# Performance work log

Measured on AMD Instinct MI355X. Metric: run time of the kernel, lower is better.

Reference implementation:

```python
import jax, jax.numpy as jnp
import numpy as np

B, S, D, H = 2, 2048, 1024, 16
DEPTH = D // H


def setup_inputs() -> dict:
    key = jax.random.key(0)
    ks = jax.random.split(key, 12)
    s = 0.02
    inp = {
        "query": jax.random.normal(ks[0], (B, S, D), jnp.float32),
        "key": jax.random.normal(ks[1], (B, S, D), jnp.float32),
        "value": jax.random.normal(ks[2], (B, S, D), jnp.float32),
        # causal mask: 1.0 where attention is disallowed (j > i)
        "mask": jnp.triu(jnp.ones((S, S), jnp.float32), k=1)[None, None, :, :],
        "wq": jax.random.normal(ks[3], (D, D), jnp.float32) * s,
        "bq": jnp.zeros((D,), jnp.float32),
        "wk": jax.random.normal(ks[4], (D, D), jnp.float32) * s,
        "bk": jnp.zeros((D,), jnp.float32),
        "wv": jax.random.normal(ks[5], (D, D), jnp.float32) * s,
        "bv": jnp.zeros((D,), jnp.float32),
        "wo": jax.random.normal(ks[6], (D, D), jnp.float32) * s,
        "bo": jnp.zeros((D,), jnp.float32),
    }
    return inp


def _split_heads(x):
    # [B,S,D] -> [B,H,S,depth]
    b, s, _ = x.shape
    return x.reshape(b, s, H, DEPTH).transpose(0, 2, 1, 3)


def reference(query, key, value, mask, wq, bq, wk, bk, wv, bv, wo, bo):
    q = _split_heads(query @ wq + bq)
    k = _split_heads(key @ wk + bk)
    v = _split_heads(value @ wv + bv)
    scale = jnp.sqrt(jnp.asarray(DEPTH, jnp.float32))
    scores = jnp.einsum("bhqd,bhkd->bhqk", q, k) / scale  # [B,H,S,S]
    scores = scores + mask * (-1e9)
    attn = jax.nn.softmax(scores, axis=-1)
    out = jnp.einsum("bhqk,bhkd->bhqd", attn, v)
    out = out.transpose(0, 2, 1, 3).reshape(query.shape[0], query.shape[1], D)
    return out @ wo + bo
```

## Files before the change

kernel.cpp:

```cpp
#include <hip/hip_runtime.h>
#include <hip/hip_bf16.h>
#include <stdint.h>
#include <math.h>

typedef float f32x4  __attribute__((ext_vector_type(4)));
typedef float f32x16 __attribute__((ext_vector_type(16)));
typedef short s16x8  __attribute__((ext_vector_type(8)));
typedef unsigned u32x4 __attribute__((ext_vector_type(4)));

#define SEQ     2048
#define DMODEL  1024
#define MROWS   4096
#define NHEAD   16

__device__ __forceinline__ unsigned short f2b(float x) {
    union { float f; unsigned u; } un; un.f = x;
    unsigned r = un.u + 0x7FFFu + ((un.u >> 16) & 1u);
    return (unsigned short)(r >> 16);
}

__device__ __forceinline__ unsigned cvtpk(float lo, float hi_) {
    unsigned r;
    asm("v_cvt_pk_bf16_f32 %0, %1, %2" : "=v"(r) : "v"(lo), "v"(hi_));
    return r;
}

#define EXP2(x) __builtin_amdgcn_exp2f(x)

__device__ __forceinline__ void g2l16(const void* g, void* l) {
    __builtin_amdgcn_global_load_lds(
        (const __attribute__((address_space(1))) unsigned int*)g,
        (__attribute__((address_space(3))) unsigned int*)l,
        16, 0, 0);
}

__global__ __launch_bounds__(256) void wtrans_kernel(
    const float* __restrict__ w0, const float* __restrict__ w1,
    const float* __restrict__ w2, const float* __restrict__ w3,
    unsigned short* __restrict__ wt)
{
    const int z = blockIdx.z;
    const float* w = z == 0 ? w0 : z == 1 ? w1 : z == 2 ? w2 : w3;
    __shared__ float t[32][33];
    const int bx = blockIdx.x * 32;
    const int by = blockIdx.y * 32;
    const int tx = threadIdx.x, ty = threadIdx.y;
    #pragma unroll
    for (int i = 0; i < 4; ++i)
        t[ty + i*8][tx] = w[(size_t)(by + ty + i*8) * DMODEL + bx + tx];
    __syncthreads();
    unsigned short* o = wt + (size_t)z * ((size_t)DMODEL * DMODEL);
    #pragma unroll
    for (int i = 0; i < 4; ++i) {
        int nrel = ty + i*8, krel = tx;
        o[(size_t)(bx + nrel) * DMODEL + by + krel] = f2b(t[krel][nrel]);
    }
}

__global__ __launch_bounds__(256, 3) void gemm_qkv_kernel(
    const float* __restrict__ qf, const float* __restrict__ kf, const float* __restrict__ vf,
    const unsigned short* __restrict__ wtbase,
    const float* __restrict__ b0, const float* __restrict__ b1, const float* __restrict__ b2,
    unsigned short* __restrict__ qh, unsigned short* __restrict__ kh,
    unsigned short* __restrict__ vT)
{
    const int mode = blockIdx.z;
    const float* Af = mode == 0 ? qf : mode == 1 ? kf : vf;
    const unsigned short* Bt = wtbase + (size_t)mode * ((size_t)DMODEL * DMODEL);
    const float* bias = mode == 0 ? b0 : mode == 1 ? b1 : b2;

    __shared__ unsigned short As[128 * 64];
    __shared__ unsigned short Bs[128 * 64];

    const int tid = threadIdx.x;
    const int lane = tid & 63, wid = tid >> 6;
    const int ll = lane & 15, lg = lane >> 4;
    const int mb = blockIdx.x * 128, nb = blockIdx.y * 128;
    const int wr = wid >> 1, wc = wid & 1;

    f32x4 acc[4][4] = {};
    f32x4 stgA[8];

    auto issueA = [&](int kb) {
        #pragma unroll
        for (int it = 0; it < 4; ++it) {
            int ci = it * 256 + tid;
            int r = ci >> 3;
            int cbs = ((ci & 7) * 16) ^ ((r & 7) << 4);
            const float* src = Af + (size_t)(mb + r) * DMODEL + kb + (cbs >> 1);
            stgA[2 * it]     = *(const f32x4*)src;
            stgA[2 * it + 1] = *(const f32x4*)(src + 4);
        }
    };

    issueA(0);

    for (int kb = 0; kb < DMODEL; kb += 64) {
        __syncthreads();
        #pragma unroll
        for (int it = 0; it < 4; ++it) {
            u32x4 w = { cvtpk(stgA[2*it][0],   stgA[2*it][1]),
                        cvtpk(stgA[2*it][2],   stgA[2*it][3]),
                        cvtpk(stgA[2*it+1][0], stgA[2*it+1][1]),
                        cvtpk(stgA[2*it+1][2], stgA[2*it+1][3]) };
            *(u32x4*)((char*)As + (it * 256 + tid) * 16) = w;
        }
        #pragma unroll
        for (int it = 0; it < 4; ++it) {
            int ci = it * 256 + tid;
            int r = ci >> 3;
            int cbs = ((ci & 7) * 16) ^ ((r & 7) << 4);
            g2l16((const char*)Bt + ((size_t)(nb + r) * DMODEL + kb) * 2 + cbs,
                  (char*)Bs + (it * 256 + wid * 64) * 16);
        }
        __syncthreads();
        if (kb + 64 < DMODEL) issueA(kb + 64);

        #pragma unroll
        for (int kk = 0; kk < 2; ++kk) {
            s16x8 af[4], bfr[4];
            #pragma unroll
            for (int m = 0; m < 4; ++m) {
                int row = wr * 64 + m * 16 + ll;
                int cbyte = (kk * 64 + lg * 16) ^ ((row & 7) << 4);
                af[m] = *(const s16x8*)((const char*)As + row * 128 + cbyte);
            }
            #pragma unroll
            for (int n = 0; n < 4; ++n) {
                int row = wc * 64 + n * 16 + ll;
                int cbyte = (kk * 64 + lg * 16) ^ ((row & 7) << 4);
                bfr[n] = *(const s16x8*)((const char*)Bs + row * 128 + cbyte);
            }
            #pragma unroll
            for (int m = 0; m < 4; ++m)
                #pragma unroll
                for (int n = 0; n < 4; ++n)
                    acc[m][n] = __builtin_amdgcn_mfma_f32_16x16x32_bf16(af[m], bfr[n], acc[m][n], 0, 0, 0);
        }
    }

    #pragma unroll
    for (int m = 0; m < 4; ++m) {
        int grow0 = mb + wr * 64 + m * 16 + lg * 4;
        #pragma unroll
        for (int n = 0; n < 4; ++n) {
            int col = nb + wc * 64 + n * 16 + ll;
            float bc = bias[col];
            f32x4 v = acc[m][n];
            if (mode == 2) {
                int b = grow0 >> 11, s0 = grow0 & 2047;
                int h = col >> 6, d = col & 63;
                ushort4 pk;
                pk.x = f2b(v[0] + bc); pk.y = f2b(v[1] + bc);
                pk.z = f2b(v[2] + bc); pk.w = f2b(v[3] + bc);
                *(ushort4*)(vT + ((size_t)((b * NHEAD + h) * 64 + d) << 11) + s0) = pk;
            } else {
                unsigned short* dst = (mode == 0) ? qh : kh;
                float scl = (mode == 0) ? 0.125f * 1.44269504089f : 1.0f;
                int b = grow0 >> 11, s0 = grow0 & 2047;
                int h = col >> 6, d = col & 63;
                #pragma unroll
                for (int r = 0; r < 4; ++r)
                    dst[((size_t)(b * NHEAD + h) * SEQ + s0 + r) * 64 + d] = f2b((v[r] + bc) * scl);
            }
        }
    }
}

__global__ __launch_bounds__(256, 2) void gemm_o_kernel(
    const unsigned short* __restrict__ Ap,
    const unsigned short* __restrict__ Bt,
    const float* __restrict__ bias,
    float* __restrict__ outF)
{
    constexpr int TM = 64;
    constexpr int WM = TM / 2;
    constexpr int MT = WM / 16;

    __shared__ unsigned short As[TM * 64];
    __shared__ unsigned short Bs[128 * 64];

    const int tid = threadIdx.x;
    const int lane = tid & 63, wid = tid >> 6;
    const int ll = lane & 15, lg = lane >> 4;
    const int mb = blockIdx.x * TM, nb = blockIdx.y * 128;
    const int wr = wid >> 1, wc = wid & 1;

    f32x4 acc[MT][4] = {};
    u32x4 stgA[2], stgB[4];

    auto issueA = [&](int kb) {
        #pragma unroll
        for (int it = 0; it < 2; ++it) {
            int ci = it * 256 + tid;
            int r = ci >> 3;
            int cbs = ((ci & 7) * 16) ^ ((r & 7) << 4);
            stgA[it] = *(const u32x4*)((const char*)Ap + ((size_t)(mb + r) * DMODEL + kb) * 2 + cbs);
        }
    };
    auto issueB = [&](int kb) {
        #pragma unroll
        for (int it = 0; it < 4; ++it) {
            int ci = it * 256 + tid;
            int r = ci >> 3;
            int cbs = ((ci & 7) * 16) ^ ((r & 7) << 4);
            stgB[it] = *(const u32x4*)((const char*)Bt + ((size_t)(nb + r) * DMODEL + kb) * 2 + cbs);
        }
    };

    issueA(0);
    issueB(0);

    for (int kb = 0; kb < DMODEL; kb += 64) {
        __syncthreads();
        #pragma unroll
        for (int it = 0; it < 2; ++it)
            *(u32x4*)((char*)As + (it * 256 + tid) * 16) = stgA[it];
        #pragma unroll
        for (int it = 0; it < 4; ++it)
            *(u32x4*)((char*)Bs + (it * 256 + tid) * 16) = stgB[it];
        __syncthreads();
        if (kb + 64 < DMODEL) { issueA(kb + 64); issueB(kb + 64); }

        #pragma unroll
        for (int kk = 0; kk < 2; ++kk) {
            s16x8 af[MT], bfr[4];
            #pragma unroll
            for (int m = 0; m < MT; ++m) {
                int row = wr * WM + m * 16 + ll;
                int cbyte = (kk * 64 + lg * 16) ^ ((row & 7) << 4);
                af[m] = *(const s16x8*)((const char*)As + row * 128 + cbyte);
            }
            #pragma unroll
            for (int n = 0; n < 4; ++n) {
                int row = wc * 64 + n * 16 + ll;
                int cbyte = (kk * 64 + lg * 16) ^ ((row & 7) << 4);
                bfr[n] = *(const s16x8*)((const char*)Bs + row * 128 + cbyte);
            }
            #pragma unroll
            for (int m = 0; m < MT; ++m)
                #pragma unroll
                for (int n = 0; n < 4; ++n)
                    acc[m][n] = __builtin_amdgcn_mfma_f32_16x16x32_bf16(af[m], bfr[n], acc[m][n], 0, 0, 0);
        }
    }

    #pragma unroll
    for (int m = 0; m < MT; ++m) {
        int grow0 = mb + wr * WM + m * 16 + lg * 4;
        #pragma unroll
        for (int n = 0; n < 4; ++n) {
            int col = nb + wc * 64 + n * 16 + ll;
            float bc = bias[col];
            f32x4 v = acc[m][n];
            #pragma unroll
            for (int r = 0; r < 4; ++r)
                outF[(size_t)(grow0 + r) * DMODEL + col] = v[r] + bc;
        }
    }
}

__global__ __launch_bounds__(256, 3) void attn_kernel(
    const unsigned short* __restrict__ qh, const unsigned short* __restrict__ kh,
    const unsigned short* __restrict__ vT, unsigned short* __restrict__ attnout)
{
    const int bid = blockIdx.x;
    const int bh = bid & 31;
    const int j  = 31 - (bid >> 5);
    const int qb = j * 64;
    const int nss = (j >> 1) + 1;

    const unsigned short* Q = qh + (size_t)bh * (SEQ * 64);
    const unsigned short* K = kh + (size_t)bh * (SEQ * 64);
    const unsigned short* V = vT + (size_t)bh * (64 * SEQ);

    __shared__ char lds[32768];
    char* Kb = lds;
    char* Vb = lds + 16384;

    const int tid = threadIdx.x, lane = tid & 63, wid = tid >> 6;
    const int l31 = lane & 31, hi = lane >> 5;
    const int qhf = wid & 1;
    const int par = wid >> 1;
    const int qrow = qb + qhf * 32 + l31;

    s16x8 aq[4];
    {
        const unsigned short* qp = Q + (size_t)qrow * 64 + hi * 8;
        #pragma unroll
        for (int u = 0; u < 4; ++u)
            aq[u] = *(const s16x8*)(qp + u * 16);
    }

    f32x16 oc0 = {}, oc1 = {};
    float mrow = -1e30f, lrow = 0.f;

    u32x4 stg[8];
    auto issue = [&](int kb) {
        #pragma unroll
        for (int it = 0; it < 4; ++it) {
            int ci = it * 256 + tid;
            int r = ci >> 3;
            int sb = ((ci & 7) * 16) ^ ((r & 7) << 4);
            stg[it] = *(const u32x4*)((const char*)K + ((size_t)(kb + r) * 64) * 2 + sb);
        }
        #pragma unroll
        for (int it = 0; it < 4; ++it) {
            int ci = it * 256 + tid;
            int d = ci >> 4;
            int sb = ((ci & 15) * 16) ^ ((d & 15) << 4);
            stg[4 + it] = *(const u32x4*)((const char*)V + (size_t)d * (SEQ * 2) + (size_t)kb * 2 + sb);
        }
    };

    issue(0);

    for (int ss = 0; ss < nss; ++ss) {
        const int kb = ss * 128;
        __syncthreads();
        #pragma unroll
        for (int it = 0; it < 8; ++it)
            *(u32x4*)(lds + it * 4096 + tid * 16) = stg[it];
        __syncthreads();
        if (ss + 1 < nss) issue(kb + 128);

        const int rb = par * 64;
        f32x16 p0 = {}, p1 = {};
        __builtin_amdgcn_s_setprio(1);
        #pragma unroll
        for (int u = 0; u < 4; ++u) {
            int r0 = rb + l31, r1 = rb + 32 + l31;
            s16x8 k0 = *(const s16x8*)(Kb + r0 * 128 + (((u * 32 + hi * 16)) ^ ((r0 & 7) << 4)));
            s16x8 k1 = *(const s16x8*)(Kb + r1 * 128 + (((u * 32 + hi * 16)) ^ ((r1 & 7) << 4)));
            p0 = __builtin_amdgcn_mfma_f32_32x32x16_bf16(k0, aq[u], p0, 0, 0, 0);
            p1 = __builtin_amdgcn_mfma_f32_32x32x16_bf16(k1, aq[u], p1, 0, 0, 0);
        }
        __builtin_amdgcn_s_setprio(0);

        if (ss == nss - 1) {
            const int pabs = kb + rb;
            #pragma unroll
            for (int r = 0; r < 16; ++r) {
                int rl = (r & 3) + 8 * (r >> 2) + 4 * hi;
                if (pabs + rl > qrow)      p0[r] = -1e30f;
                if (pabs + 32 + rl > qrow) p1[r] = -1e30f;
            }
        }

        float tm[8];
        #pragma unroll
        for (int i = 0; i < 8; ++i)
            tm[i] = fmaxf(fmaxf(p0[i], p0[i + 8]), fmaxf(p1[i], p1[i + 8]));
        float mx = fmaxf(fmaxf(fmaxf(tm[0], tm[1]), fmaxf(tm[2], tm[3])),
                         fmaxf(fmaxf(tm[4], tm[5]), fmaxf(tm[6], tm[7])));
        mx = fmaxf(mx, __shfl_xor(mx, 32, 64));

        if (!__all(mx - mrow <= 8.0f)) {
            float mnew = fmaxf(mrow, mx);
            float sclf = EXP2(mrow - mnew);
            lrow *= sclf;
            #pragma unroll
            for (int r = 0; r < 16; ++r) {
                int src = (r & 3) + 8 * (r >> 2) + 4 * hi;
                float sf = __shfl(sclf, src, 64);
                oc0[r] *= sf;
                oc1[r] *= sf;
            }
            mrow = mnew;
        }

        #pragma unroll
        for (int i = 0; i < 16; ++i) { p0[i] = EXP2(p0[i] - mrow); p1[i] = EXP2(p1[i] - mrow); }

        float s8[8];
        #pragma unroll
        for (int i = 0; i < 8; ++i)
            s8[i] = (p0[i] + p0[i + 8]) + (p1[i] + p1[i + 8]);
        float ts = ((s8[0] + s8[1]) + (s8[2] + s8[3])) + ((s8[4] + s8[5]) + (s8[6] + s8[7]));
        ts += __shfl_xor(ts, 32, 64);
        lrow += ts;

        s16x8 pa[4];
        #pragma unroll
        for (int g = 0; g < 4; ++g) {
            const f32x16 pv = (g < 2) ? p0 : p1;
            const int o = (g & 1) * 8;
            unsigned a0 = cvtpk(pv[o + 0], pv[o + 1]);
            unsigned a1 = cvtpk(pv[o + 2], pv[o + 3]);
            unsigned b0 = cvtpk(pv[o + 4], pv[o + 5]);
            unsigned b1 = cvtpk(pv[o + 6], pv[o + 7]);
            asm("v_permlane32_swap_b32 %0, %1" : "+v"(a0), "+v"(b0));
            asm("v_permlane32_swap_b32 %0, %1" : "+v"(a1), "+v"(b1));
            u32x4 t4 = {a0, a1, b0, b1};
            pa[g] = __builtin_bit_cast(s16x8, t4);
        }

        __builtin_amdgcn_s_setprio(1);
        #pragma unroll
        for (int s = 0; s < 4; ++s) {
            int cbyte = par * 128 + s * 32 + hi * 16;
            int d0 = l31, d1 = 32 + l31;
            s16x8 vb0 = *(const s16x8*)(Vb + d0 * 256 + (cbyte ^ ((d0 & 15) << 4)));
            s16x8 vb1 = *(const s16x8*)(Vb + d1 * 256 + (cbyte ^ ((d1 & 15) << 4)));
            oc0 = __builtin_amdgcn_mfma_f32_32x32x16_bf16(pa[s], vb0, oc0, 0, 0, 0);
            oc1 = __builtin_amdgcn_mfma_f32_32x32x16_bf16(pa[s], vb1, oc1, 0, 0, 0);
        }
        __builtin_amdgcn_s_setprio(0);
    }

    __syncthreads();
    float* Os = (float*)(void*)lds + qhf * 2048;
    float* ms = (float*)(void*)(lds + 16384);
    float* ls = ms + 64;
    if (par == 1) {
        if (hi == 0) { ms[qhf * 32 + l31] = mrow; ls[qhf * 32 + l31] = lrow; }
        #pragma unroll
        for (int r = 0; r < 16; ++r) {
            int rl = (r & 3) + 8 * (r >> 2) + 4 * hi;
            Os[rl * 64 + l31]      = oc0[r];
            Os[rl * 64 + 32 + l31] = oc1[r];
        }
    }
    __syncthreads();
    if (par == 0) {
        float m1 = ms[qhf * 32 + l31], l1 = ls[qhf * 32 + l31];
        float M  = fmaxf(mrow, m1);
        float wa = EXP2(mrow - M);
        float wb = EXP2(m1 - M);
        float inv = 1.0f / (lrow * wa + l1 * wb);
        const int b = bh >> 4, h = bh & 15;
        #pragma unroll
        for (int r = 0; r < 16; ++r) {
            int rl = (r & 3) + 8 * (r >> 2) + 4 * hi;
            float ar = __shfl(wa, rl, 64);
            float br = __shfl(wb, rl, 64);
            float ir = __shfl(inv, rl, 64);
            size_t base = ((size_t)(b * SEQ + qb + qhf * 32 + rl) << 10) + h * 64;
            attnout[base + l31]      = f2b((oc0[r] * ar + Os[rl * 64 + l31]      * br) * ir);
            attnout[base + 32 + l31] = f2b((oc1[r] * ar + Os[rl * 64 + 32 + l31] * br) * ir);
        }
    }
}

extern "C" void kernel_launch(void* const* d_in, const int* in_sizes, int n_in,
                              void* d_out, int out_size, void* d_ws, size_t ws_size,
                              hipStream_t stream) {
    const float* query = (const float*)d_in[0];
    const float* key   = (const float*)d_in[1];
    const float* value = (const float*)d_in[2];
    const float* wq = (const float*)d_in[4];
    const float* bq = (const float*)d_in[5];
    const float* wk = (const float*)d_in[6];
    const float* bk = (const float*)d_in[7];
    const float* wv = (const float*)d_in[8];
    const float* bv = (const float*)d_in[9];
    const float* wo = (const float*)d_in[10];
    const float* bo = (const float*)d_in[11];
    float* out = (float*)d_out;

    char* ws = (char*)d_ws;
    unsigned short* xb  = (unsigned short*)ws;
    unsigned short* wt  = (unsigned short*)(ws + 25165824);
    unsigned short* qhp = (unsigned short*)(ws + 33554432);
    unsigned short* khp = (unsigned short*)(ws + 41943040);
    unsigned short* vTp = (unsigned short*)(ws + 50331648);

    wtrans_kernel<<<dim3(32, 32, 4), dim3(32, 8), 0, stream>>>(wq, wk, wv, wo, wt);
    gemm_qkv_kernel<<<dim3(32, 8, 3), 256, 0, stream>>>(query, key, value, wt,
                                                        bq, bk, bv, qhp, khp, vTp);
    attn_kernel<<<dim3(1024), 256, 0, stream>>>(qhp, khp, vTp, xb);
    gemm_o_kernel<<<dim3(64, 8), 256, 0, stream>>>(xb, wt + 3 * (size_t)(DMODEL * DMODEL), bo, out);
}
```

Before: 97.93 us.

## Load QKV GEMM A operand directly from global into MFMA fragments, bypassing LDS

The fp32 A operand in the QKV projection GEMM is no longer staged through shared memory. Each wave now loads its own rows straight from global memory in the MFMA fragment layout and converts them to bf16 in registers. This removes the LDS writes and reads for A and halves shared memory use. In exchange, A rows are fetched redundantly by the two column waves and the previous one-step register prefetch of A is lost, so load latency is less hidden.

Result: slower. 163.6 us (+67.1%).

```diff
diff --git a/kernel.cpp b/kernel.cpp
--- a/kernel.cpp
+++ b/kernel.cpp
@@ -69,7 +69,6 @@
     const unsigned short* Bt = wtbase + (size_t)mode * ((size_t)DMODEL * DMODEL);
     const float* bias = mode == 0 ? b0 : mode == 1 ? b1 : b2;
 
-    __shared__ unsigned short As[128 * 64];
     __shared__ unsigned short Bs[128 * 64];
 
     const int tid = threadIdx.x;
@@ -79,32 +78,14 @@
     const int wr = wid >> 1, wc = wid & 1;
 
     f32x4 acc[4][4] = {};
-    f32x4 stgA[8];
-
-    auto issueA = [&](int kb) {
-        #pragma unroll
-        for (int it = 0; it < 4; ++it) {
-            int ci = it * 256 + tid;
-            int r = ci >> 3;
-            int cbs = ((ci & 7) * 16) ^ ((r & 7) << 4);
-            const float* src = Af + (size_t)(mb + r) * DMODEL + kb + (cbs >> 1);
-            stgA[2 * it]     = *(const f32x4*)src;
-            stgA[2 * it + 1] = *(const f32x4*)(src + 4);
-        }
-    };
-
-    issueA(0);
+
+    const float* arow[4];
+    #pragma unroll
+    for (int m = 0; m < 4; ++m)
+        arow[m] = Af + (size_t)(mb + wr * 64 + m * 16 + ll) * DMODEL + lg * 8;
 
     for (int kb = 0; kb < DMODEL; kb += 64) {
         __syncthreads();
-        #pragma unroll
-        for (int it = 0; it < 4; ++it) {
-            u32x4 w = { cvtpk(stgA[2*it][0],   stgA[2*it][1]),
-                        cvtpk(stgA[2*it][2],   stgA[2*it][3]),
-                        cvtpk(stgA[2*it+1][0], stgA[2*it+1][1]),
-                        cvtpk(stgA[2*it+1][2], stgA[2*it+1][3]) };
-            *(u32x4*)((char*)As + (it * 256 + tid) * 16) = w;
-        }
         #pragma unroll
         for (int it = 0; it < 4; ++it) {
             int ci = it * 256 + tid;
@@ -113,18 +94,33 @@
             g2l16((const char*)Bt + ((size_t)(nb + r) * DMODEL + kb) * 2 + cbs,
                   (char*)Bs + (it * 256 + wid * 64) * 16);
         }
-        __syncthreads();
-        if (kb + 64 < DMODEL) issueA(kb + 64);
+
+        f32x4 alo[4][2], ahi[4][2];
+        #pragma unroll
+        for (int m = 0; m < 4; ++m)
+            #pragma unroll
+            for (int kk = 0; kk < 2; ++kk) {
+                const float* ap = arow[m] + kb + kk * 32;
+                alo[m][kk] = *(const f32x4*)ap;
+                ahi[m][kk] = *(const f32x4*)(ap + 4);
+            }
+        s16x8 af[4][2];
+        #pragma unroll
+        for (int m = 0; m < 4; ++m)
+            #pragma unroll
+            for (int kk = 0; kk < 2; ++kk) {
+                u32x4 t = { cvtpk(alo[m][kk][0], alo[m][kk][1]),
+                            cvtpk(alo[m][kk][2], alo[m][kk][3]),
+                            cvtpk(ahi[m][kk][0], ahi[m][kk][1]),
+                            cvtpk(ahi[m][kk][2], ahi[m][kk][3]) };
+                af[m][kk] = __builtin_bit_cast(s16x8, t);
+            }
+
+        __syncthreads();
 
         #pragma unroll
         for (int kk = 0; kk < 2; ++kk) {
-            s16x8 af[4], bfr[4];
-            #pragma unroll
-            for (int m = 0; m < 4; ++m) {
-                int row = wr * 64 + m * 16 + ll;
-                int cbyte = (kk * 64 + lg * 16) ^ ((row & 7) << 4);
-                af[m] = *(const s16x8*)((const char*)As + row * 128 + cbyte);
-            }
+            s16x8 bfr[4];
             #pragma unroll
             for (int n = 0; n < 4; ++n) {
                 int row = wc * 64 + n * 16 + ll;
@@ -135,7 +131,7 @@
             for (int m = 0; m < 4; ++m)
                 #pragma unroll
                 for (int n = 0; n < 4; ++n)
-                    acc[m][n] = __builtin_amdgcn_mfma_f32_16x16x32_bf16(af[m], bfr[n], acc[m][n], 0, 0, 0);
+                    acc[m][n] = __builtin_amdgcn_mfma_f32_16x16x32_bf16(af[m][kk], bfr[n], acc[m][n], 0, 0, 0);
         }
     }
 
```
